# Optimization experiments

Measured on AMD Instinct MI355X. Metric: run time of the kernel, lower is better.

## Reference

```python
import jax, jax.numpy as jnp
import numpy as np

N = 648      # code length (input_size = output_size)
DV = 3       # variable degree
DC = 6       # check degree
M_PER = N // DC            # checks per layer = 108
E = N * DV                 # edges = hidden_size = 1944
BATCH = 2048
CLAMP = 0.999999


def _build_graph():
    rng = np.random.default_rng(0)
    # regular (3,6) Tanner graph via 3 permutation layers
    var_of = np.concatenate([rng.permutation(N) for _ in range(DV)])          # [E]
    chk_of = np.repeat(np.arange(DV * M_PER), DC)                              # [E]
    eye = np.eye(E, dtype=bool)
    same_chk = (chk_of[:, None] == chk_of[None, :]) & ~eye                     # extrinsic same-check
    same_var = (var_of[:, None] == var_of[None, :]) & ~eye                     # extrinsic same-var
    M_ev = np.zeros((E, N), dtype=np.float32)
    M_ev[np.arange(E), var_of] = 1.0                                           # edge -> its variable
    M_first = (same_chk.astype(np.float32) @ M_ev)                             # [E,N] CN extrinsic over vars
    M_cn = same_chk.astype(np.float32)                                         # [E,E] VN2CN_mask_CNUpdate
    M_vn = same_var.astype(np.float32)                                         # [E,E] CN2VN_mask_VNUpdate
    M_out = M_ev.T.copy()                                                      # [N,E] CN2VN_mask_output
    bias_matrix = M_ev.T.copy()                                                # [N,E] dot_bias_matrix
    return M_first, M_cn, M_vn, M_out, bias_matrix


def _xavier(key, out_f, in_f, mask):
    bound = np.sqrt(6.0 / (in_f + out_f)).astype(np.float32)
    w = jax.random.uniform(key, (out_f, in_f), jnp.float32, -bound, bound)
    return w * mask


def setup_inputs() -> dict:
    key = jax.random.key(0)
    M_first, M_cn, M_vn, M_out, bias_matrix = _build_graph()
    M_first = jnp.asarray(M_first); M_cn = jnp.asarray(M_cn)
    M_vn = jnp.asarray(M_vn); M_out = jnp.asarray(M_out)
    bias_matrix = jnp.asarray(bias_matrix)
    ks = jax.random.split(key, 6)
    x = jax.random.normal(ks[0], (BATCH, N), jnp.float32) * 2.0  # channel LLRs
    W1 = _xavier(ks[1], E, E, M_vn)
    W3 = _xavier(ks[2], E, E, M_vn)
    W5 = _xavier(ks[3], E, E, M_vn)
    W7 = _xavier(ks[4], E, E, M_vn)
    W9 = _xavier(ks[5], N, E, M_out)
    B0 = jnp.eye(N, dtype=jnp.float32); B1 = jnp.eye(N, dtype=jnp.float32)
    B2 = jnp.eye(N, dtype=jnp.float32); B3 = jnp.eye(N, dtype=jnp.float32)
    B4 = jnp.eye(N, dtype=jnp.float32)
    return {"x": x, "M_first": M_first, "M_cn": M_cn, "M_out": M_out,
            "bias_matrix": bias_matrix, "W1": W1, "W3": W3, "W5": W5,
            "W7": W7, "W9": W9, "B0": B0, "B1": B1, "B2": B2, "B3": B3, "B4": B4}


def cn_update(x, mask):
    """out[b,i] = prod over j with mask[i,j]!=0 and x[b,j]!=0 of x[b,j]; 0 if none.
    Computed in sign/log domain so it is three dense [B,in]@[in,out] matmuls
    instead of a Python loop over rows."""
    nz = x != 0.0
    logmag = jnp.log(jnp.where(nz, jnp.abs(x), 1.0))          # 0 contribution where x==0
    neg = (x < 0.0).astype(x.dtype)
    log_prod = logmag @ mask.T                                 # [B,out]
    neg_cnt = neg @ mask.T
    sign = 1.0 - 2.0 * jnp.mod(neg_cnt, 2.0)
    any_nz = (nz.astype(x.dtype) @ mask.T) > 0.0
    return jnp.where(any_nz, sign * jnp.exp(log_prod), 0.0)


def reference(x, M_first, M_cn, M_out, bias_matrix, W1, W3, W5, W7, W9,
              B0, B1, B2, B3, B4):
    llr = x                                                    # Channel_LLR [B,N]
    t = jnp.tanh(0.5 * x)
    t = jnp.clip(cn_update(t, M_first), -CLAMP, CLAMP)
    t = 2.0 * jnp.arctanh(t)
    out1 = jax.nn.sigmoid(t @ M_out.T + llr)                   # count_loss_fc: ones*mask weight, zero bias

    t = jnp.tanh(0.5 * (t @ W1.T + (llr @ B0) @ bias_matrix))
    t = jnp.clip(cn_update(t, M_cn), -CLAMP, CLAMP)
    t = 2.0 * jnp.arctanh(t)
    out2 = jax.nn.sigmoid(t @ M_out.T + llr)

    t = jnp.tanh(0.5 * (t @ W3.T + (llr @ B1) @ bias_matrix))
    t = jnp.clip(cn_update(t, M_cn), -CLAMP, CLAMP)
    t = 2.0 * jnp.arctanh(t)
    out3 = jax.nn.sigmoid(t @ M_out.T + llr)

    t = jnp.tanh(0.5 * (t @ W5.T + (llr @ B2) @ bias_matrix))
    t = jnp.clip(cn_update(t, M_cn), -CLAMP, CLAMP)
    t = 2.0 * jnp.arctanh(t)
    out4 = jax.nn.sigmoid(t @ M_out.T + llr)

    t = jnp.tanh(0.5 * (t @ W7.T + (llr @ B3) @ bias_matrix))
    t = jnp.clip(cn_update(t, M_cn), -CLAMP, CLAMP)
    t = 2.0 * jnp.arctanh(t)
    t = t @ W9.T + llr @ B4
    out5 = jax.nn.sigmoid(t)
    return (out5, out4, out3, out2, out1)
```

## Files before the change

### kernel.cpp

```cpp
#include <hip/hip_runtime.h>
#include <math.h>

#define NN 648
#define EE 1944
#define BATCH 2048
#define BS 256
#define NE_IT 8
#define TL_CLAMP 14.508648f

__device__ __forceinline__ float rcp_fast(float x) { return __builtin_amdgcn_rcpf(x); }

__device__ __forceinline__ float tanh_half(float x) {
    float E = __expf(x);
    float big = 1.0f - 2.0f * rcp_fast(E + 1.0f);
    float u = 0.5f * x;
    float small = u * (1.0f - 0.33333334f * u * u);
    return (fabsf(x) < 0.03125f) ? small : big;
}

__device__ __forceinline__ float sigm(float s) {
    return rcp_fast(1.0f + __expf(-s));
}

__global__ __launch_bounds__(BS) void extract_struct(
    const float4* __restrict__ M_out4,
    int* __restrict__ var_of, int* __restrict__ varEdge) {
    int t = blockIdx.x * BS + threadIdx.x;
    if (t >= NN * EE / 4) return;
    float4 v = M_out4[t];
    int flat = t * 4;
    int n = flat / EE;
    int e = flat - n * EE;
    if (v.x != 0.0f) { var_of[e]     = n; varEdge[n * 3 + (e)     / NN] = e;     }
    if (v.y != 0.0f) { var_of[e + 1] = n; varEdge[n * 3 + (e + 1) / NN] = e + 1; }
    if (v.z != 0.0f) { var_of[e + 2] = n; varEdge[n * 3 + (e + 2) / NN] = e + 2; }
    if (v.w != 0.0f) { var_of[e + 3] = n; varEdge[n * 3 + (e + 3) / NN] = e + 3; }
}

__global__ __launch_bounds__(BS) void extract_weights(
    const float* __restrict__ W1, const float* __restrict__ W3,
    const float* __restrict__ W5, const float* __restrict__ W7,
    const float* __restrict__ W9,
    const int* __restrict__ var_of, const int* __restrict__ varEdge,
    int2* __restrict__ nb,
    float2* __restrict__ w1v, float2* __restrict__ w3v,
    float2* __restrict__ w5v, float2* __restrict__ w7v,
    float* __restrict__ w9v) {
    int tid = blockIdx.x * BS + threadIdx.x;
    if (tid < EE) {
        int e = tid;
        int n = var_of[e];
        int e0 = varEdge[3 * n], e1 = varEdge[3 * n + 1], e2 = varEdge[3 * n + 2];
        int ea, eb;
        if (e == e0)      { ea = e1; eb = e2; }
        else if (e == e1) { ea = e0; eb = e2; }
        else              { ea = e0; eb = e1; }
        nb[e] = make_int2(ea, eb);
        size_t row = (size_t)e * EE;
        w1v[e] = make_float2(W1[row + ea], W1[row + eb]);
        w3v[e] = make_float2(W3[row + ea], W3[row + eb]);
        w5v[e] = make_float2(W5[row + ea], W5[row + eb]);
        w7v[e] = make_float2(W7[row + ea], W7[row + eb]);
    } else if (tid < EE + NN) {
        int n = tid - EE;
        #pragma unroll
        for (int k = 0; k < 3; k++) {
            int e = varEdge[3 * n + k];
            w9v[3 * n + k] = W9[(size_t)n * EE + e];
        }
    }
}


__device__ __forceinline__ void cn_pass(const float* __restrict__ te,
                                        float* __restrict__ tl, int tid) {
    #pragma unroll
    for (int i = 0; i < NE_IT; i++) {
        int e = tid + i * BS;
        if (e >= EE) break;
        int c = (int)((unsigned)e / 6u);
        const float2* p2 = (const float2*)(te + 6 * c);
        float2 v01 = p2[0], v23 = p2[1], v45 = p2[2];
        float a = te[e];
        float Q = ((v01.x * v01.y) * (v23.x * v23.y)) * (v45.x * v45.y);
        float tlv;
        if (__builtin_expect(Q != 0.0f, 1)) {
            float s = a + Q, d = a - Q;
            tlv = 0.6931472f * (__log2f(fabsf(s)) - __log2f(fabsf(d)));
            tlv = fminf(fmaxf(tlv, -TL_CLAMP), TL_CLAMP);
        } else {
            float vv[6] = {v01.x, v01.y, v23.x, v23.y, v45.x, v45.y};
            float P = 1.0f; int cz = 0;
            #pragma unroll
            for (int k = 0; k < 6; k++) {
                if (vv[k] == 0.0f) cz++; else P *= vv[k];
            }
            float ext;
            if (a != 0.0f) ext = (cz >= 5) ? 0.0f : P * rcp_fast(a);
            else           ext = (cz >= 6) ? 0.0f : P;
            ext = fminf(fmaxf(ext, -0.999999f), 0.999999f);
            tlv = 0.6931472f * __log2f((1.0f + ext) * rcp_fast(1.0f - ext));
        }
        tl[e] = tlv;
    }
}

__device__ __forceinline__ void marg_out(float* __restrict__ dst,
        const float* __restrict__ tl, const float* __restrict__ llr_s,
        const int* __restrict__ varEdge, int tid) {
    for (int n = tid; n < NN; n += BS) {
        float s = llr_s[n] + tl[varEdge[3 * n]] + tl[varEdge[3 * n + 1]]
                           + tl[varEdge[3 * n + 2]];
        dst[n] = sigm(s);
    }
}

__global__ __launch_bounds__(BS, 8) void bp_main(
    const float* __restrict__ x,
    const int* __restrict__ var_of, const int* __restrict__ varEdge,
    const int2* __restrict__ nb,
    const float2* __restrict__ w1v, const float2* __restrict__ w3v,
    const float2* __restrict__ w5v, const float2* __restrict__ w7v,
    const float* __restrict__ w9v,
    float* __restrict__ out) {
    __shared__ __align__(16) float llr_s[NN];
    __shared__ __align__(16) float te[EE];
    __shared__ __align__(16) float tl[EE];
    const int b = blockIdx.x;
    const int tid = threadIdx.x;

    const float* xr = x + (size_t)b * NN;
    for (int n = tid; n < NN; n += BS) llr_s[n] = xr[n];
    __syncthreads();

    float lb[NE_IT];
    const float* pA[NE_IT];
    const float* pB[NE_IT];
    #pragma unroll
    for (int i = 0; i < NE_IT; i++) {
        int e = tid + i * BS;
        if (e < EE) {
            lb[i] = llr_s[var_of[e]];
            int2 nn = nb[e];
            pA[i] = tl + nn.x;
            pB[i] = tl + nn.y;
            te[e] = tanh_half(lb[i]);
        } else {
            lb[i] = 0.0f; pA[i] = tl; pB[i] = tl;
        }
    }
    __syncthreads();
    cn_pass(te, tl, tid);
    __syncthreads();
    marg_out(out + ((size_t)(4 * BATCH) + b) * NN, tl, llr_s, varEdge, tid);

    const float2* wvs[4] = {w1v, w3v, w5v, w7v};
    for (int L = 0; L < 4; L++) {
        const float2* __restrict__ wv = wvs[L];
        #pragma unroll
        for (int i = 0; i < NE_IT; i++) {
            int e = tid + i * BS;
            if (e < EE) {
                float2 w = wv[e];
                float pre = fmaf(w.x, *pA[i], fmaf(w.y, *pB[i], lb[i]));
                te[e] = tanh_half(pre);
            }
        }
        __syncthreads();
        cn_pass(te, tl, tid);
        __syncthreads();
        if (L < 3) {
            marg_out(out + ((size_t)((3 - L) * BATCH) + b) * NN, tl, llr_s, varEdge, tid);
        } else {
            for (int n = tid; n < NN; n += BS) {
                float s = llr_s[n]
                        + w9v[3 * n]     * tl[varEdge[3 * n]]
                        + w9v[3 * n + 1] * tl[varEdge[3 * n + 1]]
                        + w9v[3 * n + 2] * tl[varEdge[3 * n + 2]];
                out[(size_t)b * NN + n] = sigm(s);
            }
        }
    }
}

extern "C" void kernel_launch(void* const* d_in, const int* in_sizes, int n_in,
                              void* d_out, int out_size, void* d_ws, size_t ws_size,
                              hipStream_t stream) {
    const float* x     = (const float*)d_in[0];
    const float* M_out = (const float*)d_in[3];
    const float* W1    = (const float*)d_in[5];
    const float* W3    = (const float*)d_in[6];
    const float* W5    = (const float*)d_in[7];
    const float* W7    = (const float*)d_in[8];
    const float* W9    = (const float*)d_in[9];
    float* out = (float*)d_out;

    char* ws = (char*)d_ws;
    int2*   nb      = (int2*)ws;   ws += EE * 8;
    float2* w1v     = (float2*)ws; ws += EE * 8;
    float2* w3v     = (float2*)ws; ws += EE * 8;
    float2* w5v     = (float2*)ws; ws += EE * 8;
    float2* w7v     = (float2*)ws; ws += EE * 8;
    int*    var_of  = (int*)ws;    ws += EE * 4;
    int*    varEdge = (int*)ws;    ws += NN * 3 * 4;
    float*  w9v     = (float*)ws;  ws += NN * 3 * 4;

    const int tot4 = NN * EE / 4;
    extract_struct<<<(tot4 + BS - 1) / BS, BS, 0, stream>>>(
        (const float4*)M_out, var_of, varEdge);
    extract_weights<<<(EE + NN + BS - 1) / BS, BS, 0, stream>>>(
        W1, W3, W5, W7, W9, var_of, varEdge, nb, w1v, w3v, w5v, w7v, w9v);
    bp_main<<<BATCH, BS, 0, stream>>>(
        x, var_of, varEdge, nb, w1v, w3v, w5v, w7v, w9v, out);
}
```

Measured before the change: 177.8 us.

## Process edge pairs per thread and cache variable-edge indices in registers

Each thread now handles two adjacent edges (972 pairs instead of 1944 edges). Within a check the pair shares one 6-way product, and weights, neighbour indices and LLRs are fetched with float4/int4/float2 loads. varEdge indices for the marginal outputs are loaded into registers once instead of every layer. The rare zero-product fallback moves into a noinline function to keep register pressure down. The extraction kernel is also spread across four times as many threads, one weight matrix each.

```diff
diff --git a/kernel.cpp b/kernel.cpp
--- a/kernel.cpp
+++ b/kernel.cpp
@@ -3,9 +3,10 @@
 
 #define NN 648
 #define EE 1944
+#define NP 972
 #define BATCH 2048
 #define BS 256
-#define NE_IT 8
+#define NP_IT 4
 #define TL_CLAMP 14.508648f
 
 __device__ __forceinline__ float rcp_fast(float x) { return __builtin_amdgcn_rcpf(x); }
@@ -20,6 +21,26 @@
 
 __device__ __forceinline__ float sigm(float s) {
     return rcp_fast(1.0f + __expf(-s));
+}
+
+__device__ __noinline__ float cn_fallback(float a, const float2 v01,
+                                          const float2 v23, const float2 v45) {
+    float vv[6] = {v01.x, v01.y, v23.x, v23.y, v45.x, v45.y};
+    float P = 1.0f; int cz = 0;
+    #pragma unroll
+    for (int k = 0; k < 6; k++) {
+        if (vv[k] == 0.0f) cz++; else P *= vv[k];
+    }
+    float ext;
+    if (a != 0.0f) ext = (cz >= 5) ? 0.0f : P * rcp_fast(a);
+    else           ext = (cz >= 6) ? 0.0f : P;
+    ext = fminf(fmaxf(ext, -0.999999f), 0.999999f);
+    return 0.6931472f * __log2f((1.0f + ext) * rcp_fast(1.0f - ext));
+}
+
+__device__ __forceinline__ float cn_edge(float a, float Q) {
+    float t = 0.6931472f * (__log2f(fabsf(a + Q)) - __log2f(fabsf(a - Q)));
+    return fminf(fmaxf(t, -TL_CLAMP), TL_CLAMP);
 }
 
 __global__ __launch_bounds__(BS) void extract_struct(
@@ -42,27 +63,28 @@
     const float* __restrict__ W5, const float* __restrict__ W7,
     const float* __restrict__ W9,
     const int* __restrict__ var_of, const int* __restrict__ varEdge,
-    int2* __restrict__ nb,
-    float2* __restrict__ w1v, float2* __restrict__ w3v,
-    float2* __restrict__ w5v, float2* __restrict__ w7v,
+    int4* __restrict__ nbq,
+    float4* __restrict__ w1q, float4* __restrict__ w3q,
+    float4* __restrict__ w5q, float4* __restrict__ w7q,
     float* __restrict__ w9v) {
-    int tid = blockIdx.x * BS + threadIdx.x;
-    if (tid < EE) {
-        int e = tid;
+    int t = blockIdx.x * BS + threadIdx.x;
+    if (t < 4 * EE) {
+        int m = t / EE;
+        int e = t - m * EE;
         int n = var_of[e];
         int e0 = varEdge[3 * n], e1 = varEdge[3 * n + 1], e2 = varEdge[3 * n + 2];
         int ea, eb;
         if (e == e0)      { ea = e1; eb = e2; }
         else if (e == e1) { ea = e0; eb = e2; }
         else              { ea = e0; eb = e1; }
-        nb[e] = make_int2(ea, eb);
+        const float* W = (m == 0) ? W1 : (m == 1) ? W3 : (m == 2) ? W5 : W7;
         size_t row = (size_t)e * EE;
-        w1v[e] = make_float2(W1[row + ea], W1[row + eb]);
-        w3v[e] = make_float2(W3[row + ea], W3[row + eb]);
-        w5v[e] = make_float2(W5[row + ea], W5[row + eb]);
-        w7v[e] = make_float2(W7[row + ea], W7[row + eb]);
-    } else if (tid < EE + NN) {
-        int n = tid - EE;
+        float2 w = make_float2(W[row + ea], W[row + eb]);
+        float4* dq = (m == 0) ? w1q : (m == 1) ? w3q : (m == 2) ? w5q : w7q;
+        ((float2*)dq)[e] = w;
+        if (m == 0) ((int2*)nbq)[e] = make_int2(ea, eb);
+    } else if (t < 4 * EE + NN) {
+        int n = t - 4 * EE;
         #pragma unroll
         for (int k = 0; k < 3; k++) {
             int e = varEdge[3 * n + k];
@@ -71,56 +93,13 @@
     }
 }
 
-
-__device__ __forceinline__ void cn_pass(const float* __restrict__ te,
-                                        float* __restrict__ tl, int tid) {
-    #pragma unroll
-    for (int i = 0; i < NE_IT; i++) {
-        int e = tid + i * BS;
-        if (e >= EE) break;
-        int c = (int)((unsigned)e / 6u);
-        const float2* p2 = (const float2*)(te + 6 * c);
-        float2 v01 = p2[0], v23 = p2[1], v45 = p2[2];
-        float a = te[e];
-        float Q = ((v01.x * v01.y) * (v23.x * v23.y)) * (v45.x * v45.y);
-        float tlv;
-        if (__builtin_expect(Q != 0.0f, 1)) {
-            float s = a + Q, d = a - Q;
-            tlv = 0.6931472f * (__log2f(fabsf(s)) - __log2f(fabsf(d)));
-            tlv = fminf(fmaxf(tlv, -TL_CLAMP), TL_CLAMP);
-        } else {
-            float vv[6] = {v01.x, v01.y, v23.x, v23.y, v45.x, v45.y};
-            float P = 1.0f; int cz = 0;
-            #pragma unroll
-            for (int k = 0; k < 6; k++) {
-                if (vv[k] == 0.0f) cz++; else P *= vv[k];
-            }
-            float ext;
-            if (a != 0.0f) ext = (cz >= 5) ? 0.0f : P * rcp_fast(a);
-            else           ext = (cz >= 6) ? 0.0f : P;
-            ext = fminf(fmaxf(ext, -0.999999f), 0.999999f);
-            tlv = 0.6931472f * __log2f((1.0f + ext) * rcp_fast(1.0f - ext));
-        }
-        tl[e] = tlv;
-    }
-}
-
-__device__ __forceinline__ void marg_out(float* __restrict__ dst,
-        const float* __restrict__ tl, const float* __restrict__ llr_s,
-        const int* __restrict__ varEdge, int tid) {
-    for (int n = tid; n < NN; n += BS) {
-        float s = llr_s[n] + tl[varEdge[3 * n]] + tl[varEdge[3 * n + 1]]
-                           + tl[varEdge[3 * n + 2]];
-        dst[n] = sigm(s);
-    }
-}
-
 __global__ __launch_bounds__(BS, 8) void bp_main(
     const float* __restrict__ x,
-    const int* __restrict__ var_of, const int* __restrict__ varEdge,
-    const int2* __restrict__ nb,
-    const float2* __restrict__ w1v, const float2* __restrict__ w3v,
-    const float2* __restrict__ w5v, const float2* __restrict__ w7v,
+    const int2* __restrict__ var2,
+    const int* __restrict__ varEdge,
+    const int4* __restrict__ nbq,
+    const float4* __restrict__ w1q, const float4* __restrict__ w3q,
+    const float4* __restrict__ w5q, const float4* __restrict__ w7q,
     const float* __restrict__ w9v,
     float* __restrict__ out) {
     __shared__ __align__(16) float llr_s[NN];
@@ -133,51 +112,99 @@
     for (int n = tid; n < NN; n += BS) llr_s[n] = xr[n];
     __syncthreads();
 
-    float lb[NE_IT];
-    const float* pA[NE_IT];
-    const float* pB[NE_IT];
+    float2 lb[NP_IT];
+    int oA[NP_IT], oB[NP_IT], oC[NP_IT], oD[NP_IT];
+    int cOff[NP_IT];
     #pragma unroll
-    for (int i = 0; i < NE_IT; i++) {
-        int e = tid + i * BS;
-        if (e < EE) {
-            lb[i] = llr_s[var_of[e]];
-            int2 nn = nb[e];
-            pA[i] = tl + nn.x;
-            pB[i] = tl + nn.y;
-            te[e] = tanh_half(lb[i]);
+    for (int i = 0; i < NP_IT; i++) {
+        int p = tid + i * BS;
+        if (p < NP) {
+            int2 v = var2[p];
+            lb[i] = make_float2(llr_s[v.x], llr_s[v.y]);
+            int4 nn = nbq[p];
+            oA[i] = nn.x; oB[i] = nn.y; oC[i] = nn.z; oD[i] = nn.w;
+            cOff[i] = ((unsigned)p / 3u) * 6;
+            *(float2*)(te + 2 * p) = make_float2(tanh_half(lb[i].x),
+                                                 tanh_half(lb[i].y));
         } else {
-            lb[i] = 0.0f; pA[i] = tl; pB[i] = tl;
-        }
+            lb[i] = make_float2(0.f, 0.f);
+            oA[i] = oB[i] = oC[i] = oD[i] = 0; cOff[i] = 0;
+        }
+    }
+    int m0[3], m1[3], m2[3];
+    #pragma unroll
+    for (int j = 0; j < 3; j++) {
+        int n = tid + j * BS;
+        if (n < NN) {
+            m0[j] = varEdge[3 * n]; m1[j] = varEdge[3 * n + 1];
+            m2[j] = varEdge[3 * n + 2];
+        } else { m0[j] = m1[j] = m2[j] = 0; }
     }
     __syncthreads();
-    cn_pass(te, tl, tid);
+
+    auto cn_pass = [&]() {
+        #pragma unroll
+        for (int i = 0; i < NP_IT; i++) {
+            int p = tid + i * BS;
+            if (p >= NP) break;
+            const float2* ck = (const float2*)(te + cOff[i]);
+            float2 v01 = ck[0], v23 = ck[1], v45 = ck[2];
+            float2 a = *(const float2*)(te + 2 * p);
+            float Q = ((v01.x * v01.y) * (v23.x * v23.y)) * (v45.x * v45.y);
+            float t0, t1;
+            if (__builtin_expect(Q != 0.0f, 1)) {
+                t0 = cn_edge(a.x, Q);
+                t1 = cn_edge(a.y, Q);
+            } else {
+                t0 = cn_fallback(a.x, v01, v23, v45);
+                t1 = cn_fallback(a.y, v01, v23, v45);
+            }
+            *(float2*)(tl + 2 * p) = make_float2(t0, t1);
+        }
+    };
+    auto marg_out = [&](float* dst) {
+        #pragma unroll
+        for (int j = 0; j < 3; j++) {
+            int n = tid + j * BS;
+            if (n < NN)
+                dst[n] = sigm(llr_s[n] + tl[m0[j]] + tl[m1[j]] + tl[m2[j]]);
+        }
+    };
+
+    cn_pass();
     __syncthreads();
-    marg_out(out + ((size_t)(4 * BATCH) + b) * NN, tl, llr_s, varEdge, tid);
-
-    const float2* wvs[4] = {w1v, w3v, w5v, w7v};
+    marg_out(out + ((size_t)(4 * BATCH) + b) * NN);
+
+    const float4* wqs[4] = {w1q, w3q, w5q, w7q};
     for (int L = 0; L < 4; L++) {
-        const float2* __restrict__ wv = wvs[L];
-        #pragma unroll
-        for (int i = 0; i < NE_IT; i++) {
-            int e = tid + i * BS;
-            if (e < EE) {
-                float2 w = wv[e];
-                float pre = fmaf(w.x, *pA[i], fmaf(w.y, *pB[i], lb[i]));
-                te[e] = tanh_half(pre);
+        const float4* __restrict__ wq = wqs[L];
+        #pragma unroll
+        for (int i = 0; i < NP_IT; i++) {
+            int p = tid + i * BS;
+            if (p < NP) {
+                float4 w = wq[p];
+                float preX = fmaf(w.x, tl[oA[i]], fmaf(w.y, tl[oB[i]], lb[i].x));
+                float preY = fmaf(w.z, tl[oC[i]], fmaf(w.w, tl[oD[i]], lb[i].y));
+                *(float2*)(te + 2 * p) = make_float2(tanh_half(preX),
+                                                     tanh_half(preY));
             }
         }
         __syncthreads();
-        cn_pass(te, tl, tid);
+        cn_pass();
         __syncthreads();
         if (L < 3) {
-            marg_out(out + ((size_t)((3 - L) * BATCH) + b) * NN, tl, llr_s, varEdge, tid);
+            marg_out(out + ((size_t)((3 - L) * BATCH) + b) * NN);
         } else {
-            for (int n = tid; n < NN; n += BS) {
-                float s = llr_s[n]
-                        + w9v[3 * n]     * tl[varEdge[3 * n]]
-                        + w9v[3 * n + 1] * tl[varEdge[3 * n + 1]]
-                        + w9v[3 * n + 2] * tl[varEdge[3 * n + 2]];
-                out[(size_t)b * NN + n] = sigm(s);
+            #pragma unroll
+            for (int j = 0; j < 3; j++) {
+                int n = tid + j * BS;
+                if (n < NN) {
+                    float s = llr_s[n]
+                            + w9v[3 * n]     * tl[m0[j]]
+                            + w9v[3 * n + 1] * tl[m1[j]]
+                            + w9v[3 * n + 2] * tl[m2[j]];
+                    out[(size_t)b * NN + n] = sigm(s);
+                }
             }
         }
     }
@@ -196,11 +223,11 @@
     float* out = (float*)d_out;
 
     char* ws = (char*)d_ws;
-    int2*   nb      = (int2*)ws;   ws += EE * 8;
-    float2* w1v     = (float2*)ws; ws += EE * 8;
-    float2* w3v     = (float2*)ws; ws += EE * 8;
-    float2* w5v     = (float2*)ws; ws += EE * 8;
-    float2* w7v     = (float2*)ws; ws += EE * 8;
+    int4*   nbq     = (int4*)ws;   ws += NP * 16;
+    float4* w1q     = (float4*)ws; ws += NP * 16;
+    float4* w3q     = (float4*)ws; ws += NP * 16;
+    float4* w5q     = (float4*)ws; ws += NP * 16;
+    float4* w7q     = (float4*)ws; ws += NP * 16;
     int*    var_of  = (int*)ws;    ws += EE * 4;
     int*    varEdge = (int*)ws;    ws += NN * 3 * 4;
     float*  w9v     = (float*)ws;  ws += NN * 3 * 4;
@@ -208,8 +235,9 @@
     const int tot4 = NN * EE / 4;
     extract_struct<<<(tot4 + BS - 1) / BS, BS, 0, stream>>>(
         (const float4*)M_out, var_of, varEdge);
-    extract_weights<<<(EE + NN + BS - 1) / BS, BS, 0, stream>>>(
-        W1, W3, W5, W7, W9, var_of, varEdge, nb, w1v, w3v, w5v, w7v, w9v);
+    const int totW = 4 * EE + NN;
+    extract_weights<<<(totW + BS - 1) / BS, BS, 0, stream>>>(
+        W1, W3, W5, W7, W9, var_of, varEdge, nbq, w1q, w3q, w5q, w7q, w9v);
     bp_main<<<BATCH, BS, 0, stream>>>(
-        x, var_of, varEdge, nb, w1v, w3v, w5v, w7v, w9v, out);
-}
+        x, (const int2*)var_of, varEdge, nbq, w1q, w3q, w5q, w7q, w9v, out);
+}
```

Measured after the change: 175.7 us. Within noise of the previous version (-1.2%).
